# Kernel optimization log

Measured on AMD Instinct MI355X. Metric: run time of the kernel, lower is better.

Reference implementation:

```python
import jax, jax.numpy as jnp
import numpy as np

HIDDEN = 512
INPUT = 512


def setup_inputs() -> dict:
    key = jax.random.key(0)
    ks = jax.random.split(key, 13)
    stdv = 1.0 / np.sqrt(HIDDEN)
    u = lambda k, shape: jax.random.uniform(k, shape, jnp.float32, -stdv, stdv)
    inp = {"x": jax.random.normal(ks[0], (64, 1024, INPUT), jnp.float32)}
    names = ["W_i", "U_i", "b_i", "W_f", "U_f", "b_f", "W_c", "U_c", "b_c", "W_o", "U_o", "b_o"]
    shapes = [(INPUT, HIDDEN), (HIDDEN, HIDDEN), (HIDDEN,)] * 4
    for n, s, k in zip(names, shapes, ks[1:]):
        inp[n] = u(k, s)
    return inp


def reference(x, W_i, U_i, b_i, W_f, U_f, b_f, W_c, U_c, b_c, W_o, U_o, b_o):
    bs, seq, _ = x.shape
    hs = U_i.shape[0]
    # Precompute input projections for all timesteps (batched GEMM), then scan the recurrence.
    # Stack 4 gates: [seq, bs, 4*hs]
    W = jnp.concatenate([W_i, W_f, W_c, W_o], axis=1)          # [in, 4h]
    U = jnp.concatenate([U_i, U_f, U_c, U_o], axis=1)          # [h, 4h]
    b = jnp.concatenate([b_i, b_f, b_c, b_o], axis=0)          # [4h]
    x_proj = jnp.einsum('bsi,ih->sbh', x, W) + b               # [seq, bs, 4h]

    def step(carry, xp):
        h, c = carry
        z = xp + h @ U                                          # [bs, 4h]
        i = jax.nn.relu(z[:, 0*hs:1*hs])
        f = jax.nn.relu(z[:, 1*hs:2*hs])
        g = jnp.tanh(z[:, 2*hs:3*hs])
        o = jax.nn.sigmoid(z[:, 3*hs:4*hs])
        c = f * c + i * g
        h = o * jnp.tanh(c)
        return (h, c), h

    h0 = jnp.zeros((bs, hs), x.dtype)
    c0 = jnp.zeros((bs, hs), x.dtype)
    (_, _), hs_seq = jax.lax.scan(step, (h0, c0), x_proj)       # [seq, bs, h]
    return jnp.transpose(hs_seq, (1, 0, 2))                     # [bs, seq, h]
```

## Files before the change

### kernel.cpp

```cpp
#include <hip/hip_runtime.h>
#include <hip/hip_bf16.h>
#include <stdint.h>

typedef float  f32x4  __attribute__((ext_vector_type(4)));
typedef short  bf16x8 __attribute__((ext_vector_type(8)));
typedef unsigned int  u32;
typedef unsigned short u16;
typedef unsigned long long u64;

#define BS    64
#define SEQ   1024
#define HID   512

__device__ __forceinline__ u16 f2bf(float f) {
    u32 u = __float_as_uint(f);
    u32 r = (u + 0x7FFFu + ((u >> 16) & 1u)) >> 16;
    return (u16)r;
}
__device__ __forceinline__ float bf2f(u16 h) {
    return __uint_as_float(((u32)h) << 16);
}
__device__ __forceinline__ u32 pk2(float a, float b) {
    return (u32)f2bf(a) | ((u32)f2bf(b) << 16);
}
__device__ __forceinline__ float sigm(float x)  { return 1.f / (1.f + __expf(-x)); }
__device__ __forceinline__ float tanh_(float x) { return 1.f - 2.f / (1.f + __expf(2.f * x)); }

#define OFF_W4T   0
#define OFF_B4    (2u*1024*1024)
#define OFF_HB    (OFF_B4 + 8192)
#define OFF_TG    (OFF_HB + 262144)
#define OFF_CBUF  (OFF_TG + 4096)
#define OFF_XP    (4u*1024*1024)

__global__ void pack_w(const float* __restrict__ Wi, const float* __restrict__ Wf,
                       const float* __restrict__ Wc, const float* __restrict__ Wo,
                       const float* __restrict__ bi, const float* __restrict__ bf_,
                       const float* __restrict__ bc, const float* __restrict__ bo,
                       u16* __restrict__ w4t, float* __restrict__ b4) {
    int n = blockIdx.x;
    int gate = n >> 9, c = n & 511;
    const float* W = (gate == 0) ? Wi : (gate == 1) ? Wf : (gate == 2) ? Wc : Wo;
    const float* B = (gate == 0) ? bi : (gate == 1) ? bf_ : (gate == 2) ? bc : bo;
    int k = threadIdx.x * 2;
    u32 v = pk2(W[(size_t)k * 512 + c], W[(size_t)(k + 1) * 512 + c]);
    *(u32*)&w4t[(size_t)n * 512 + k] = v;
    if (threadIdx.x == 0) b4[n] = B[c];
}

__global__ __launch_bounds__(256, 2)
void gemm_proj(const float* __restrict__ x, const u16* __restrict__ w4t,
               const float* __restrict__ b4, u16* __restrict__ xp,
               int t0, int Tc) {
    __shared__ __align__(16) u16 lA[128 * 64];
    __shared__ __align__(16) u16 lB[128 * 64];

    int ntb = blockIdx.x & 15;
    int mb  = blockIdx.x >> 4;
    int tps = Tc >> 7;
    int bstrip = mb / tps, tb = mb % tps;
    const float* Abase = x + (size_t)(bstrip * SEQ + t0 + tb * 128) * 512;
    size_t xprow0 = (size_t)bstrip * Tc + tb * 128;
    int n0 = ntb * 128;

    int tid = threadIdx.x, lane = tid & 63, w = tid >> 6;
    int wm = w >> 1, wn = w & 1;

    f32x4 acc[4][4];
#pragma unroll
    for (int a = 0; a < 4; a++)
#pragma unroll
        for (int b = 0; b < 4; b++) acc[a][b] = (f32x4){0.f, 0.f, 0.f, 0.f};

    for (int kb = 0; kb < 8; kb++) {
        {
            int row = tid >> 1, half = tid & 1;
            const float* src = Abase + (size_t)row * 512 + kb * 64 + half * 32;
            u32 tmp[16];
#pragma unroll
            for (int q = 0; q < 8; q++) {
                float4 f = *(const float4*)(src + q * 4);
                tmp[q * 2]     = pk2(f.x, f.y);
                tmp[q * 2 + 1] = pk2(f.z, f.w);
            }
            u16* dst = &lA[row * 64 + half * 32];
#pragma unroll
            for (int q = 0; q < 4; q++)
                *(uint4*)(dst + q * 8) = *(uint4*)&tmp[q * 4];
        }
        {
            int row = tid >> 1, kc = (tid & 1) * 32;
            const u16* src = w4t + (size_t)(n0 + row) * 512 + kb * 64 + kc;
            uint4 v0 = *(const uint4*)(src);
            uint4 v1 = *(const uint4*)(src + 8);
            uint4 v2 = *(const uint4*)(src + 16);
            uint4 v3 = *(const uint4*)(src + 24);
            u16* dst = &lB[row * 64 + kc];
            *(uint4*)(dst) = v0; *(uint4*)(dst + 8) = v1;
            *(uint4*)(dst + 16) = v2; *(uint4*)(dst + 24) = v3;
        }
        __syncthreads();
#pragma unroll
        for (int kt = 0; kt < 2; kt++) {
            bf16x8 a[4], bb[4];
#pragma unroll
            for (int mt = 0; mt < 4; mt++)
                a[mt] = *(const bf16x8*)&lA[(wm * 64 + mt * 16 + (lane & 15)) * 64 + kt * 32 + (lane >> 4) * 8];
#pragma unroll
            for (int nt = 0; nt < 4; nt++)
                bb[nt] = *(const bf16x8*)&lB[(wn * 64 + nt * 16 + (lane & 15)) * 64 + kt * 32 + (lane >> 4) * 8];
#pragma unroll
            for (int mt = 0; mt < 4; mt++)
#pragma unroll
                for (int nt = 0; nt < 4; nt++)
                    acc[mt][nt] = __builtin_amdgcn_mfma_f32_16x16x32_bf16(a[mt], bb[nt], acc[mt][nt], 0, 0, 0);
        }
        __syncthreads();
    }
#pragma unroll
    for (int nt = 0; nt < 4; nt++) {
        int n = n0 + wn * 64 + nt * 16 + (lane & 15);
        float bv = b4[n];
#pragma unroll
        for (int mt = 0; mt < 4; mt++)
#pragma unroll
            for (int r = 0; r < 4; r++) {
                size_t m = xprow0 + wm * 64 + mt * 16 + (lane >> 4) * 4 + r;
                xp[m * 2048 + n] = f2bf(acc[mt][nt][r] + bv);
            }
    }
}

__global__ __launch_bounds__(256, 1)
void lstm_rec(const float* __restrict__ U0, const float* __restrict__ U1,
              const float* __restrict__ U2, const float* __restrict__ U3,
              const u16* __restrict__ xp, float* __restrict__ out,
              u64* __restrict__ hb, u32* __restrict__ tg,
              float* __restrict__ cbuf, int t0, int Tc) {
    const int gid = blockIdx.x >> 3;
    const int q   = blockIdx.x & 7;
    const int tid = threadIdx.x;
    const int w = tid >> 6, lane = tid & 63;
    const int col16 = lane & 15;
    const int krow  = lane >> 4;
    const int mycol = q * 64 + w * 16 + col16;

    __shared__ __align__(16) u16 h_lds[2][16 * 512];

    const float* Ug[4] = {U0, U1, U2, U3};
    bf16x8 ub[16][4];
#pragma unroll
    for (int kt = 0; kt < 16; kt++) {
        int kbase = kt * 32 + krow * 8;
#pragma unroll
        for (int g = 0; g < 4; g++) {
            union { u16 sh[8]; bf16x8 v; } uu;
#pragma unroll
            for (int j = 0; j < 8; j++)
                uu.sh[j] = f2bf(Ug[g][(size_t)(kbase + j) * 512 + mycol]);
            ub[kt][g] = uu.v;
        }
    }

    float c[4];
    if (t0 == 0) {
        c[0] = c[1] = c[2] = c[3] = 0.f;
    } else {
#pragma unroll
        for (int r = 0; r < 4; r++)
            c[r] = cbuf[((size_t)gid * 16 + krow * 4 + r) * 512 + mycol];
    }

    const u64* tagp = (const u64*)(tg + gid * 16);

    for (int tl = 0; tl < Tc; tl++) {
        const int t = t0 + tl;

        u16 xr[4][4];
#pragma unroll
        for (int g = 0; g < 4; g++)
#pragma unroll
            for (int r = 0; r < 4; r++)
                xr[g][r] = xp[(size_t)((gid * 16 + krow * 4 + r) * Tc + tl) * 2048
                              + g * 512 + mycol];

        {
            const u32 te = (u32)t;
            for (;;) {
                u64 a0 = __hip_atomic_load(tagp + 0, __ATOMIC_RELAXED, __HIP_MEMORY_SCOPE_AGENT);
                u64 a1 = __hip_atomic_load(tagp + 1, __ATOMIC_RELAXED, __HIP_MEMORY_SCOPE_AGENT);
                u64 a2 = __hip_atomic_load(tagp + 2, __ATOMIC_RELAXED, __HIP_MEMORY_SCOPE_AGENT);
                u64 a3 = __hip_atomic_load(tagp + 3, __ATOMIC_RELAXED, __HIP_MEMORY_SCOPE_AGENT);
                bool ok = ((u32)a0 >= te) & ((u32)(a0 >> 32) >= te)
                        & ((u32)a1 >= te) & ((u32)(a1 >> 32) >= te)
                        & ((u32)a2 >= te) & ((u32)(a2 >> 32) >= te)
                        & ((u32)a3 >= te) & ((u32)(a3 >> 32) >= te);
                if (ok) break;
            }
        }

        u64 v[16];
        {
            const u64* src = hb + (((size_t)((t + 1) & 1)) << 14) + ((size_t)gid << 12) + tid;
            const u32 te = (u32)t & 0xFFFFu;
            for (;;) {
#pragma unroll
                for (int j = 0; j < 16; j++)
                    v[j] = __hip_atomic_load(src + j * 256, __ATOMIC_RELAXED,
                                             __HIP_MEMORY_SCOPE_AGENT);
                u32 bad = 0;
#pragma unroll
                for (int j = 0; j < 16; j++) {
                    bad |= (((u32)v[j]) ^ te) & 0xFFFFu;
                    bad |= (((u32)(v[j] >> 32)) ^ te) & 0xFFFFu;
                }
                if (!bad) break;
            }
        }

        u16* hl = &h_lds[t & 1][0];
#pragma unroll
        for (int j = 0; j < 16; j++) {
            u32 packed = ((u32)v[j] >> 16) | ((u32)(v[j] >> 32) & 0xFFFF0000u);
            u32 byte = ((u32)(j * 1024) + (u32)(tid * 4)) ^ ((u32)(j & 7) << 4);
            *(u32*)((char*)hl + byte) = packed;
        }
        __syncthreads();

        f32x4 acc[4];
#pragma unroll
        for (int g = 0; g < 4; g++) acc[g] = (f32x4){0.f, 0.f, 0.f, 0.f};
#pragma unroll
        for (int kt = 0; kt < 16; kt++) {
            u32 byte = ((u32)(col16 * 1024) + (u32)(kt * 64) + (u32)(krow * 16))
                       ^ ((u32)(col16 & 7) << 4);
            bf16x8 af = *(const bf16x8*)((const char*)hl + byte);
#pragma unroll
            for (int g = 0; g < 4; g++)
                acc[g] = __builtin_amdgcn_mfma_f32_16x16x32_bf16(af, ub[kt][g], acc[g], 0, 0, 0);
        }

        float hv[4];
#pragma unroll
        for (int r = 0; r < 4; r++) {
            float zi = acc[0][r] + bf2f(xr[0][r]);
            float zf = acc[1][r] + bf2f(xr[1][r]);
            float zg = acc[2][r] + bf2f(xr[2][r]);
            float zo = acc[3][r] + bf2f(xr[3][r]);
            float iv = fmaxf(zi, 0.f), fv = fmaxf(zf, 0.f);
            float gv = tanh_(zg), ov = sigm(zo);
            c[r] = fv * c[r] + iv * gv;
            hv[r] = ov * tanh_(c[r]);
        }

        {
            const u32 tag = (u32)((t + 1) & 0xFFFF);
            u32* dst = (u32*)(hb + (((size_t)(t & 1) * 4 + gid) << 12));
#pragma unroll
            for (int r = 0; r < 4; r++) {
                int row = krow * 4 + r;
                u32 word = ((u32)f2bf(hv[r]) << 16) | tag;
                __hip_atomic_store(dst + row * 512 + mycol, word, __ATOMIC_RELAXED,
                                   __HIP_MEMORY_SCOPE_AGENT);
            }
            if (tid == 0)
                __hip_atomic_store(tg + gid * 16 + q, (u32)(t + 1),
                                   __ATOMIC_RELAXED, __HIP_MEMORY_SCOPE_AGENT);
        }

#pragma unroll
        for (int r = 0; r < 4; r++)
            out[(size_t)((gid * 16 + krow * 4 + r) * SEQ + t) * 512 + mycol] = hv[r];
    }

#pragma unroll
    for (int r = 0; r < 4; r++)
        cbuf[((size_t)gid * 16 + krow * 4 + r) * 512 + mycol] = c[r];
}

extern "C" void kernel_launch(void* const* d_in, const int* in_sizes, int n_in,
                              void* d_out, int out_size, void* d_ws, size_t ws_size,
                              hipStream_t stream) {
    const float* x  = (const float*)d_in[0];
    const float* Wg[4] = {(const float*)d_in[1], (const float*)d_in[4],
                          (const float*)d_in[7], (const float*)d_in[10]};
    const float* Ug[4] = {(const float*)d_in[2], (const float*)d_in[5],
                          (const float*)d_in[8], (const float*)d_in[11]};
    const float* Bg[4] = {(const float*)d_in[3], (const float*)d_in[6],
                          (const float*)d_in[9], (const float*)d_in[12]};
    float* out = (float*)d_out;

    char* ws = (char*)d_ws;
    u16*   w4t   = (u16*)(ws + OFF_W4T);
    float* b4    = (float*)(ws + OFF_B4);
    u64*   hb    = (u64*)(ws + OFF_HB);
    u32*   tg    = (u32*)(ws + OFF_TG);
    float* cbuf  = (float*)(ws + OFF_CBUF);
    u16*   xp    = (u16*)(ws + OFF_XP);

    int Tc = 128;
    for (int c = 1024; c >= 128; c >>= 1)
        if ((size_t)OFF_XP + (size_t)BS * c * 2048 * 2 <= ws_size) { Tc = c; break; }

    hipMemsetAsync(ws + OFF_HB, 0, 262144 + 4096, stream);

    pack_w<<<2048, 256, 0, stream>>>(Wg[0], Wg[1], Wg[2], Wg[3],
                                     Bg[0], Bg[1], Bg[2], Bg[3], w4t, b4);

    for (int t0 = 0; t0 < SEQ; t0 += Tc) {
        dim3 ggrid((unsigned)(BS * (Tc / 128) * 16));
        gemm_proj<<<ggrid, 256, 0, stream>>>(x, w4t, b4, xp, t0, Tc);
        lstm_rec<<<32, 256, 0, stream>>>(Ug[0], Ug[1], Ug[2], Ug[3],
                                         xp, out, hb, tg, cbuf, t0, Tc);
    }
}
```

Measured before the change: 4.186 ms.

## Overlap next-chunk input projection GEMM with recurrence in a fused kernel

Splits the sequence into 64-step chunks and launches one fused kernel per chunk. In it, 32 blocks run the LSTM recurrence on the current chunk while the other blocks compute the input projection for the next chunk into a double-buffered workspace. The aim is to hide the projection GEMM behind the latency-bound recurrence, which only occupies a few CUs. It also drops the separate per-block tag spin (relying on tagged h words alone), adds s_sleep in the poll loop, and uses 64-row GEMM tiles. The costs are more kernel launches and per-chunk reloading of U into registers, and the GEMM blocks may contend with the recurrence blocks for memory bandwidth.

```diff
diff --git a/kernel.cpp b/kernel.cpp
--- a/kernel.cpp
+++ b/kernel.cpp
@@ -11,6 +11,7 @@
 #define BS    64
 #define SEQ   1024
 #define HID   512
+#define TCH   64
 
 __device__ __forceinline__ u16 f2bf(float f) {
     u32 u = __float_as_uint(f);
@@ -29,9 +30,9 @@
 #define OFF_W4T   0
 #define OFF_B4    (2u*1024*1024)
 #define OFF_HB    (OFF_B4 + 8192)
-#define OFF_TG    (OFF_HB + 262144)
-#define OFF_CBUF  (OFF_TG + 4096)
-#define OFF_XP    (4u*1024*1024)
+#define OFF_CBUF  (OFF_HB + 262144)
+#define OFF_XP0   (4u*1024*1024)
+#define OFF_XP1   (20u*1024*1024)
 
 __global__ void pack_w(const float* __restrict__ Wi, const float* __restrict__ Wf,
                        const float* __restrict__ Wc, const float* __restrict__ Wo,
@@ -48,45 +49,40 @@
     if (threadIdx.x == 0) b4[n] = B[c];
 }
 
-__global__ __launch_bounds__(256, 2)
-void gemm_proj(const float* __restrict__ x, const u16* __restrict__ w4t,
-               const float* __restrict__ b4, u16* __restrict__ xp,
-               int t0, int Tc) {
-    __shared__ __align__(16) u16 lA[128 * 64];
-    __shared__ __align__(16) u16 lB[128 * 64];
-
-    int ntb = blockIdx.x & 15;
-    int mb  = blockIdx.x >> 4;
-    int tps = Tc >> 7;
-    int bstrip = mb / tps, tb = mb % tps;
-    const float* Abase = x + (size_t)(bstrip * SEQ + t0 + tb * 128) * 512;
-    size_t xprow0 = (size_t)bstrip * Tc + tb * 128;
+__device__ __forceinline__ void gemm64_role(int g, const float* __restrict__ x,
+                                            const u16* __restrict__ w4t,
+                                            const float* __restrict__ b4,
+                                            u16* __restrict__ xpn, int t0n,
+                                            char* smem) {
+    u16* lA = (u16*)smem;
+    u16* lB = (u16*)(smem + 8192);
+    int ntb = g & 15, bstrip = g >> 4;
+    const float* Abase = x + (size_t)(bstrip * SEQ + t0n) * 512;
     int n0 = ntb * 128;
 
     int tid = threadIdx.x, lane = tid & 63, w = tid >> 6;
     int wm = w >> 1, wn = w & 1;
 
-    f32x4 acc[4][4];
-#pragma unroll
-    for (int a = 0; a < 4; a++)
+    f32x4 acc[2][4];
+#pragma unroll
+    for (int a = 0; a < 2; a++)
 #pragma unroll
         for (int b = 0; b < 4; b++) acc[a][b] = (f32x4){0.f, 0.f, 0.f, 0.f};
 
     for (int kb = 0; kb < 8; kb++) {
         {
-            int row = tid >> 1, half = tid & 1;
-            const float* src = Abase + (size_t)row * 512 + kb * 64 + half * 32;
-            u32 tmp[16];
-#pragma unroll
-            for (int q = 0; q < 8; q++) {
-                float4 f = *(const float4*)(src + q * 4);
-                tmp[q * 2]     = pk2(f.x, f.y);
-                tmp[q * 2 + 1] = pk2(f.z, f.w);
+            int row = tid >> 2, qd = tid & 3;
+            const float* src = Abase + (size_t)row * 512 + kb * 64 + qd * 16;
+            u32 tmp[8];
+#pragma unroll
+            for (int qq = 0; qq < 4; qq++) {
+                float4 f = *(const float4*)(src + qq * 4);
+                tmp[qq * 2]     = pk2(f.x, f.y);
+                tmp[qq * 2 + 1] = pk2(f.z, f.w);
             }
-            u16* dst = &lA[row * 64 + half * 32];
-#pragma unroll
-            for (int q = 0; q < 4; q++)
-                *(uint4*)(dst + q * 8) = *(uint4*)&tmp[q * 4];
+            u16* dst = &lA[row * 64 + qd * 16];
+            *(uint4*)(dst)     = *(uint4*)&tmp[0];
+            *(uint4*)(dst + 8) = *(uint4*)&tmp[4];
         }
         {
             int row = tid >> 1, kc = (tid & 1) * 32;
@@ -102,15 +98,15 @@
         __syncthreads();
 #pragma unroll
         for (int kt = 0; kt < 2; kt++) {
-            bf16x8 a[4], bb[4];
-#pragma unroll
-            for (int mt = 0; mt < 4; mt++)
-                a[mt] = *(const bf16x8*)&lA[(wm * 64 + mt * 16 + (lane & 15)) * 64 + kt * 32 + (lane >> 4) * 8];
+            bf16x8 a[2], bb[4];
+#pragma unroll
+            for (int mt = 0; mt < 2; mt++)
+                a[mt] = *(const bf16x8*)&lA[(wm * 32 + mt * 16 + (lane & 15)) * 64 + kt * 32 + (lane >> 4) * 8];
 #pragma unroll
             for (int nt = 0; nt < 4; nt++)
                 bb[nt] = *(const bf16x8*)&lB[(wn * 64 + nt * 16 + (lane & 15)) * 64 + kt * 32 + (lane >> 4) * 8];
 #pragma unroll
-            for (int mt = 0; mt < 4; mt++)
+            for (int mt = 0; mt < 2; mt++)
 #pragma unroll
                 for (int nt = 0; nt < 4; nt++)
                     acc[mt][nt] = __builtin_amdgcn_mfma_f32_16x16x32_bf16(a[mt], bb[nt], acc[mt][nt], 0, 0, 0);
@@ -122,21 +118,24 @@
         int n = n0 + wn * 64 + nt * 16 + (lane & 15);
         float bv = b4[n];
 #pragma unroll
-        for (int mt = 0; mt < 4; mt++)
+        for (int mt = 0; mt < 2; mt++)
 #pragma unroll
             for (int r = 0; r < 4; r++) {
-                size_t m = xprow0 + wm * 64 + mt * 16 + (lane >> 4) * 4 + r;
-                xp[m * 2048 + n] = f2bf(acc[mt][nt][r] + bv);
+                size_t m = (size_t)bstrip * TCH + wm * 32 + mt * 16 + (lane >> 4) * 4 + r;
+                xpn[m * 2048 + n] = f2bf(acc[mt][nt][r] + bv);
             }
     }
 }
 
-__global__ __launch_bounds__(256, 1)
-void lstm_rec(const float* __restrict__ U0, const float* __restrict__ U1,
-              const float* __restrict__ U2, const float* __restrict__ U3,
-              const u16* __restrict__ xp, float* __restrict__ out,
-              u64* __restrict__ hb, u32* __restrict__ tg,
-              float* __restrict__ cbuf, int t0, int Tc) {
+__device__ __forceinline__ void rec_role(const float* __restrict__ U0,
+                                         const float* __restrict__ U1,
+                                         const float* __restrict__ U2,
+                                         const float* __restrict__ U3,
+                                         const u16* __restrict__ xpc,
+                                         float* __restrict__ out,
+                                         u64* __restrict__ hb,
+                                         float* __restrict__ cbuf,
+                                         int t0, char* smem) {
     const int gid = blockIdx.x >> 3;
     const int q   = blockIdx.x & 7;
     const int tid = threadIdx.x;
@@ -145,7 +144,7 @@
     const int krow  = lane >> 4;
     const int mycol = q * 64 + w * 16 + col16;
 
-    __shared__ __align__(16) u16 h_lds[2][16 * 512];
+    u16* h_lds = (u16*)smem;
 
     const float* Ug[4] = {U0, U1, U2, U3};
     bf16x8 ub[16][4];
@@ -171,9 +170,7 @@
             c[r] = cbuf[((size_t)gid * 16 + krow * 4 + r) * 512 + mycol];
     }
 
-    const u64* tagp = (const u64*)(tg + gid * 16);
-
-    for (int tl = 0; tl < Tc; tl++) {
+    for (int tl = 0; tl < TCH; tl++) {
         const int t = t0 + tl;
 
         u16 xr[4][4];
@@ -181,23 +178,8 @@
         for (int g = 0; g < 4; g++)
 #pragma unroll
             for (int r = 0; r < 4; r++)
-                xr[g][r] = xp[(size_t)((gid * 16 + krow * 4 + r) * Tc + tl) * 2048
-                              + g * 512 + mycol];
-
-        {
-            const u32 te = (u32)t;
-            for (;;) {
-                u64 a0 = __hip_atomic_load(tagp + 0, __ATOMIC_RELAXED, __HIP_MEMORY_SCOPE_AGENT);
-                u64 a1 = __hip_atomic_load(tagp + 1, __ATOMIC_RELAXED, __HIP_MEMORY_SCOPE_AGENT);
-                u64 a2 = __hip_atomic_load(tagp + 2, __ATOMIC_RELAXED, __HIP_MEMORY_SCOPE_AGENT);
-                u64 a3 = __hip_atomic_load(tagp + 3, __ATOMIC_RELAXED, __HIP_MEMORY_SCOPE_AGENT);
-                bool ok = ((u32)a0 >= te) & ((u32)(a0 >> 32) >= te)
-                        & ((u32)a1 >= te) & ((u32)(a1 >> 32) >= te)
-                        & ((u32)a2 >= te) & ((u32)(a2 >> 32) >= te)
-                        & ((u32)a3 >= te) & ((u32)(a3 >> 32) >= te);
-                if (ok) break;
-            }
-        }
+                xr[g][r] = xpc[(size_t)((gid * 16 + krow * 4 + r) * TCH + tl) * 2048
+                               + g * 512 + mycol];
 
         u64 v[16];
         {
@@ -215,10 +197,11 @@
                     bad |= (((u32)(v[j] >> 32)) ^ te) & 0xFFFFu;
                 }
                 if (!bad) break;
+                __builtin_amdgcn_s_sleep(6);
             }
         }
 
-        u16* hl = &h_lds[t & 1][0];
+        u16* hl = h_lds + (t & 1) * 8192;
 #pragma unroll
         for (int j = 0; j < 16; j++) {
             u32 packed = ((u32)v[j] >> 16) | ((u32)(v[j] >> 32) & 0xFFFF0000u);
@@ -263,9 +246,6 @@
                 __hip_atomic_store(dst + row * 512 + mycol, word, __ATOMIC_RELAXED,
                                    __HIP_MEMORY_SCOPE_AGENT);
             }
-            if (tid == 0)
-                __hip_atomic_store(tg + gid * 16 + q, (u32)(t + 1),
-                                   __ATOMIC_RELAXED, __HIP_MEMORY_SCOPE_AGENT);
         }
 
 #pragma unroll
@@ -276,6 +256,29 @@
 #pragma unroll
     for (int r = 0; r < 4; r++)
         cbuf[((size_t)gid * 16 + krow * 4 + r) * 512 + mycol] = c[r];
+}
+
+__global__ __launch_bounds__(256, 2)
+void gemm_boot(const float* __restrict__ x, const u16* __restrict__ w4t,
+               const float* __restrict__ b4, u16* __restrict__ xpn, int t0n) {
+    __shared__ __align__(16) char smem[24576];
+    gemm64_role(blockIdx.x, x, w4t, b4, xpn, t0n, smem);
+}
+
+__global__ __launch_bounds__(256, 1)
+void fused_step(const float* __restrict__ U0, const float* __restrict__ U1,
+                const float* __restrict__ U2, const float* __restrict__ U3,
+                const float* __restrict__ x, const u16* __restrict__ w4t,
+                const float* __restrict__ b4,
+                const u16* __restrict__ xpc, u16* __restrict__ xpn,
+                float* __restrict__ out, u64* __restrict__ hb,
+                float* __restrict__ cbuf, int t0) {
+    __shared__ __align__(16) char smem[32768];
+    if (blockIdx.x < 32) {
+        rec_role(U0, U1, U2, U3, xpc, out, hb, cbuf, t0, smem);
+    } else {
+        gemm64_role((int)blockIdx.x - 32, x, w4t, b4, xpn, t0 + TCH, smem);
+    }
 }
 
 extern "C" void kernel_launch(void* const* d_in, const int* in_sizes, int n_in,
@@ -294,23 +297,24 @@
     u16*   w4t   = (u16*)(ws + OFF_W4T);
     float* b4    = (float*)(ws + OFF_B4);
     u64*   hb    = (u64*)(ws + OFF_HB);
-    u32*   tg    = (u32*)(ws + OFF_TG);
     float* cbuf  = (float*)(ws + OFF_CBUF);
-    u16*   xp    = (u16*)(ws + OFF_XP);
-
-    int Tc = 128;
-    for (int c = 1024; c >= 128; c >>= 1)
-        if ((size_t)OFF_XP + (size_t)BS * c * 2048 * 2 <= ws_size) { Tc = c; break; }
-
-    hipMemsetAsync(ws + OFF_HB, 0, 262144 + 4096, stream);
+    u16*   xp0   = (u16*)(ws + OFF_XP0);
+    u16*   xp1   = (u16*)(ws + OFF_XP1);
+
+    hipMemsetAsync(ws + OFF_HB, 0, 262144, stream);
 
     pack_w<<<2048, 256, 0, stream>>>(Wg[0], Wg[1], Wg[2], Wg[3],
                                      Bg[0], Bg[1], Bg[2], Bg[3], w4t, b4);
 
-    for (int t0 = 0; t0 < SEQ; t0 += Tc) {
-        dim3 ggrid((unsigned)(BS * (Tc / 128) * 16));
-        gemm_proj<<<ggrid, 256, 0, stream>>>(x, w4t, b4, xp, t0, Tc);
-        lstm_rec<<<32, 256, 0, stream>>>(Ug[0], Ug[1], Ug[2], Ug[3],
-                                         xp, out, hb, tg, cbuf, t0, Tc);
-    }
-}
+    const int nch = SEQ / TCH;
+    gemm_boot<<<64 * 16, 256, 0, stream>>>(x, w4t, b4, xp0, 0);
+
+    for (int ci = 0; ci < nch; ci++) {
+        u16* xpc = (ci & 1) ? xp1 : xp0;
+        u16* xpn = (ci & 1) ? xp0 : xp1;
+        int  nb  = 32 + ((ci + 1 < nch) ? 64 * 16 : 0);
+        fused_step<<<nb, 256, 0, stream>>>(Ug[0], Ug[1], Ug[2], Ug[3],
+                                           x, w4t, b4, xpc, xpn,
+                                           out, hb, cbuf, ci * TCH);
+    }
+}
```

Result: faster. 3.993 ms (-4.6%).
